# Kernel optimization log

Measured on AMD Instinct MI355X. Metric: run time of the kernel, lower is better.

## Reference

```python
import jax, jax.numpy as jnp
import numpy as np

B, H, F, Z = 256, 2048, 1024, 512
T, PREV, TS = 16, 16, 32  # predicted_visit, previous_visit, time_step


def _relu_dense(x, W, b):
    return jax.nn.relu(x @ W + b)


def setup_inputs() -> dict:
    key = jax.random.key(0)
    ks = jax.random.split(key, 40)
    def rn(i, shape, scale=0.02):
        return jax.random.normal(ks[i], shape, jnp.float32) * scale
    D = H + F + Z  # LSTM input dim: concat(z_j, h_i, y_j_)
    inp = {
        'h_i': jax.random.normal(ks[0], (B, H), jnp.float32),
        # increasing visit times so Hawkes exp(past - current) stays bounded
        'input_t': jnp.cumsum(jax.random.uniform(ks[1], (B, TS), jnp.float32), axis=1) * 0.1,
        'Wk': rn(2, (D, 4 * H)),
        'Wr': rn(3, (H, 4 * H)),
        'b_lstm': jnp.zeros((4 * H,), jnp.float32),
    }
    dense_dims = [(H, F), (F, F), (F, F), (2 * H + 2 * F, Z), (Z, Z), (Z, Z), (2 * H + F, Z), (Z, Z), (Z, Z)]
    for n, (di, do) in enumerate(dense_dims, start=1):
        inp['W%d' % n] = rn(3 + n, (di, do))
        inp['b%d' % n] = jnp.zeros((do,), jnp.float32)
    for n, name in enumerate(['alpha', 'beta', 'base', 'tw']):
        inp[name] = jax.random.uniform(ks[20 + n], (1, 1), jnp.float32) * 0.05
    inp['noise_inf'] = jax.random.normal(ks[30], (T, B, Z), jnp.float32)
    inp['noise_prior'] = jax.random.normal(ks[31], (T, B, Z), jnp.float32)
    return inp


def reference(h_i, input_t, Wk, Wr, b_lstm, W1, b1, W2, b2, W3, b3, W4, b4, W5, b5, W6, b6, W7, b7, W8, b8, W9, b9, alpha, beta, base, tw, noise_inf, noise_prior):
    # ---- Hawkes intensity for every decode step (vectorized over steps) ----
    idxs = PREV + jnp.arange(T)                        # current_time_index per step j
    cur_t = input_t[:, idxs]                           # [B, T]
    diff = input_t[:, None, :] - cur_t[:, :, None]     # [B, T, TS] = past - current
    mask = jnp.arange(TS)[None, None, :] < idxs[None, :, None]
    trig = jnp.sum(jnp.where(mask, jnp.exp(diff), 0.0), axis=-1)   # [B, T]
    lam = base[0, 0] + alpha[0, 0] * beta[0, 0] * trig             # conditional intensity [B, T]
    # original: softplus(matmul(tile(lam,[1,H]), tile(tw,[H,1]))) == softplus(lam * H * tw)
    delta_t = jnp.log1p(jnp.exp(lam * (H * tw[0, 0])))             # [B, T]
    time_est = cur_t + delta_t                                     # [B, T]

    def step(carry, xs):
        h, c, y_prev, z_prev = carry
        lam_j, n_inf, n_pri = xs
        x = jnp.concatenate([z_prev, h_i, y_prev], axis=1)         # [B, Z+H+F]
        gates = x @ Wk + h @ Wr + b_lstm                           # [B, 4H]
        i_g, f_g, g_g, o_g = jnp.split(gates, 4, axis=1)           # keras gate order i,f,c,o
        c_new = jax.nn.sigmoid(f_g) * c + jax.nn.sigmoid(i_g) * jnp.tanh(g_g)
        h_new = jax.nn.sigmoid(o_g) * jnp.tanh(c_new)
        # Original code indexes keras state as c=state[0](=h_new), h_=state[1](=c_new):
        # s_j fed to the VAE nets is the CELL state, and the intensity scales the cell
        # that is carried to the next step, while h carried is the unscaled h_new.
        s_j = c_new
        c_next = lam_j[:, None] * c_new
        y = _relu_dense(_relu_dense(_relu_dense(h_new, W1, b1), W2, b2), W3, b3)
        hz = _relu_dense(jnp.concatenate([h_i, s_j, y, y_prev], axis=1), W4, b4)
        mean = _relu_dense(hz, W5, b5)
        logv = _relu_dense(hz, W6, b6)
        z = mean + n_inf * jnp.sqrt(jnp.exp(logv))
        hz_p = _relu_dense(jnp.concatenate([h_i, s_j, y_prev], axis=1), W7, b7)
        mean_p = _relu_dense(hz_p, W8, b8)
        logv_p = _relu_dense(hz_p, W9, b9)
        z_p = mean_p + n_pri * jnp.sqrt(jnp.exp(logv_p))
        return (h_new, c_next, y, z), (y, mean, logv, z, z_p)

    carry0 = (jnp.zeros((B, H), h_i.dtype), jnp.zeros((B, H), h_i.dtype),
              jnp.zeros((B, F), h_i.dtype), jnp.zeros((B, Z), h_i.dtype))
    xs = (lam.T, noise_inf, noise_prior)  # leading axis = decode step
    _, (ys, means, logvs, zs, zps) = jax.lax.scan(step, carry0, xs)
    tb = lambda a: jnp.transpose(a, (1, 0, 2))    # [T,B,*] -> [B,T,*]
    input_t_all = cur_t.T.reshape(-1, 1)          # matches per-step concat of [B,1]
    time_estimates = time_est.T.reshape(-1, 1)
    return (tb(ys), tb(means), tb(logvs), tb(zs), tb(zps), input_t_all, time_estimates)
```

## Files before the change

### kernel.cpp

```cpp
#include <hip/hip_runtime.h>
#include <stdint.h>

typedef unsigned short u16;
typedef __bf16 bf16x8 __attribute__((ext_vector_type(8)));
typedef float f32x4 __attribute__((ext_vector_type(4)));

static constexpr int NB  = 256;
static constexpr int NH  = 2048;
static constexpr int NF  = 1024;
static constexpr int NZ  = 512;
static constexpr int NT  = 16;
static constexpr int NTS = 32;
static constexpr int NG4 = 8192;
static constexpr int NBLK = 256;

__device__ __forceinline__ u16 f2bf(float f) {
  union { float f; uint32_t u; } x; x.f = f;
  uint32_t r = x.u + 0x7fffu + ((x.u >> 16) & 1u);
  return (u16)(r >> 16);
}
__device__ __forceinline__ float sigm(float x) { return 1.f / (1.f + expf(-x)); }

__device__ __forceinline__ void gload16(const void* g, void* l) {
  __builtin_amdgcn_global_load_lds(
      (__attribute__((address_space(1))) void*)const_cast<void*>(g),
      (__attribute__((address_space(3))) void*)l, 16, 0, 0);
}

__device__ __forceinline__ unsigned aload(const unsigned* p) {
  return __hip_atomic_load(p, __ATOMIC_RELAXED, __HIP_MEMORY_SCOPE_AGENT);
}
__device__ __forceinline__ void astore(unsigned* p, unsigned v) {
  __hip_atomic_store(p, v, __ATOMIC_RELAXED, __HIP_MEMORY_SCOPE_AGENT);
}
__device__ __forceinline__ void t_st(float* p, float v) {
  __hip_atomic_store(p, v, __ATOMIC_RELAXED, __HIP_MEMORY_SCOPE_AGENT);
}
__device__ __forceinline__ void t_st32(uint32_t* p, uint32_t v) {
  __hip_atomic_store(p, v, __ATOMIC_RELAXED, __HIP_MEMORY_SCOPE_AGENT);
}

__device__ __forceinline__ void tl4(const float* p, f32x4& v) {
  asm volatile("global_load_dwordx4 %0, %1, off sc0 sc1" : "=&v"(v) : "v"(p));
}
__device__ __forceinline__ void ts2(void* p, uint32_t lo, uint32_t hi) {
  uint2 d; d.x = lo; d.y = hi;
  asm volatile("global_store_dwordx2 %0, %1, off sc0 sc1" :: "v"(p), "v"(d) : "memory");
}
__device__ __forceinline__ void t_wait() {
  asm volatile("s_waitcnt vmcnt(0)" ::: "memory");
  __builtin_amdgcn_sched_barrier(0);
}

__device__ __forceinline__ void gsync(unsigned* flags, unsigned* rel, unsigned& epoch) {
  ++epoch;
  asm volatile("s_waitcnt vmcnt(0)" ::: "memory");
  __syncthreads();
  if (blockIdx.x == 0) {
    if (threadIdx.x > 0)
      while (aload(&flags[threadIdx.x]) < epoch) __builtin_amdgcn_s_sleep(1);
    __syncthreads();
    if (threadIdx.x == 0) astore(rel, epoch);
  } else if (threadIdx.x == 0) {
    astore(&flags[blockIdx.x], epoch);
    while (aload(rel) < epoch) __builtin_amdgcn_s_sleep(1);
  }
  __syncthreads();
}

template<int F>
__device__ __forceinline__ void gemm_core(const u16* __restrict__ A, const u16* __restrict__ W,
                                          int lda, int ldw, int niter, int wg,
                                          char* lds, f32x4 (&acc)[F][4]) {
  constexpr int BUF = F * 4096 + 4096;
  const int tid = threadIdx.x, lane = tid & 63, wave = tid >> 6;
  const int srow = lane >> 2;
  const int schunk = (((lane & 3) ^ ((lane >> 3) & 3)) << 3);
  const u16* ga = A + (size_t)(wave * (F * 16) + srow) * lda + schunk;
  const u16* gw = W + (size_t)(wave * wg + srow) * ldw + schunk;
  const size_t astep = (size_t)16 * lda;
  auto STAGE = [&](int idx) {
    const int koff = idx << 5;
    char* base = lds + (idx % 3) * BUF;
    char* ad = base + wave * (F * 1024);
#pragma unroll
    for (int k = 0; k < F; ++k) gload16(ga + koff + k * astep, ad + k * 1024);
    gload16(gw + koff, base + F * 4096 + wave * 1024);
  };
  int rA[F], rW[4];
  const int b15 = lane & 15, h4 = lane >> 4, rx = (b15 >> 1) & 3;
#pragma unroll
  for (int f = 0; f < F; ++f) rA[f] = (wave * (F * 16) + f * 16 + b15) * 64 + ((h4 ^ rx) << 4);
#pragma unroll
  for (int q = 0; q < 4; ++q) rW[q] = F * 4096 + (q * 16 + b15) * 64 + ((h4 ^ rx) << 4);

  const int npro = niter < 3 ? niter : 3;
  for (int j = 0; j < npro; ++j) STAGE(j);
  for (int i = 0; i < niter; ++i) {
    const int ahead = niter - 1 - i;
    if constexpr (F == 4) {
      if (ahead >= 2)      asm volatile("s_waitcnt vmcnt(10)" ::: "memory");
      else if (ahead == 1) asm volatile("s_waitcnt vmcnt(5)" ::: "memory");
      else                 asm volatile("s_waitcnt vmcnt(0)" ::: "memory");
    } else if constexpr (F == 2) {
      if (ahead >= 2)      asm volatile("s_waitcnt vmcnt(6)" ::: "memory");
      else if (ahead == 1) asm volatile("s_waitcnt vmcnt(3)" ::: "memory");
      else                 asm volatile("s_waitcnt vmcnt(0)" ::: "memory");
    } else {
      if (ahead >= 2)      asm volatile("s_waitcnt vmcnt(4)" ::: "memory");
      else if (ahead == 1) asm volatile("s_waitcnt vmcnt(2)" ::: "memory");
      else                 asm volatile("s_waitcnt vmcnt(0)" ::: "memory");
    }
    __builtin_amdgcn_sched_barrier(0);
    asm volatile("s_barrier" ::: "memory");
    __builtin_amdgcn_sched_barrier(0);
    const char* base = lds + (i % 3) * BUF;
    bf16x8 av[F], bv[4];
#pragma unroll
    for (int f = 0; f < F; ++f) av[f] = *(const bf16x8*)(base + rA[f]);
#pragma unroll
    for (int q = 0; q < 4; ++q) bv[q] = *(const bf16x8*)(base + rW[q]);
    asm volatile("s_waitcnt lgkmcnt(0)" ::: "memory");
    __builtin_amdgcn_sched_barrier(0);
    asm volatile("s_barrier" ::: "memory");
    __builtin_amdgcn_sched_barrier(0);
    if (i + 3 < niter) STAGE(i + 3);
#pragma unroll
    for (int f = 0; f < F; ++f)
#pragma unroll
      for (int q = 0; q < 4; ++q)
        acc[f][q] = __builtin_amdgcn_mfma_f32_16x16x32_bf16(av[f], bv[q], acc[f][q], 0, 0, 0);
  }
}

__device__ __forceinline__ void flush_u16(const char* tb, u16* dst, int rs, int m0, int n0) {
  __syncthreads();
  const int tid = threadIdx.x, row = tid >> 2, qt = tid & 3;
  const uint2* s = (const uint2*)(tb + row * 128 + qt * 32);
  u16* d = dst + (size_t)(m0 + row) * rs + n0 + qt * 16;
  ts2(d, s[0].x, s[0].y);
  ts2(d + 4, s[1].x, s[1].y);
  ts2(d + 8, s[2].x, s[2].y);
  ts2(d + 12, s[3].x, s[3].y);
}
__device__ __forceinline__ void flush_f32(const char* tb, float* dst, int rs, int m0, int n0) {
  __syncthreads();
  const int tid = threadIdx.x, row = tid >> 2, qt = tid & 3;
  const uint2* s = (const uint2*)(tb + row * 256 + qt * 64);
  float* d = dst + (size_t)(m0 + row) * rs + n0 + qt * 16;
#pragma unroll
  for (int i = 0; i < 8; ++i) ts2(d + i * 2, s[i].x, s[i].y);
}

__device__ __forceinline__ void wbias(float* of, const float* bias, int Nn, int n0,
                                      const f32x4 (&acc)[4][4]) {
  const int tid = threadIdx.x, lane = tid & 63, wave = tid >> 6;
  const int b15 = lane & 15, h4 = lane >> 4;
#pragma unroll
  for (int q = 0; q < 4; ++q) {
    const int n = n0 + q * 16 + b15;
    const float bb = bias[n];
#pragma unroll
    for (int f = 0; f < 4; ++f) {
      const int m = wave * 64 + f * 16 + h4 * 4;
#pragma unroll
      for (int r = 0; r < 4; ++r) t_st(&of[(size_t)(m + r) * Nn + n], acc[f][q][r] + bb);
    }
  }
}

struct TJobs {
  const float* W[13]; u16* D[13];
  int N[13], klo[13], ntx[13], base[14];
  const float* h_i; u16* hi_bf; int hi_base;
};
__global__ __launch_bounds__(256) void setup_tr(TJobs j) {
  const int bid = blockIdx.x, t = threadIdx.x;
  if (bid >= j.hi_base) {
    int i = ((bid - j.hi_base) * 256 + t) * 4;
    float4 v = *(const float4*)(j.h_i + i);
    ushort4 o; o.x = f2bf(v.x); o.y = f2bf(v.y); o.z = f2bf(v.z); o.w = f2bf(v.w);
    *(ushort4*)(j.hi_bf + i) = o;
    return;
  }
  int k = 0;
  while (bid >= j.base[k + 1]) ++k;
  const int tix = bid - j.base[k];
  const int ntx = j.ntx[k];
  const int kk0 = (tix % ntx) * 32, n0 = (tix / ntx) * 32;
  const int N = j.N[k], k_lo = j.klo[k], k_len = ntx * 32;
  const float* W = j.W[k];
  u16* WT = j.D[k];
  __shared__ float tile[32][33];
  const int r = t >> 3, cg = t & 7;
  const float4 v = *(const float4*)(W + (size_t)(k_lo + kk0 + r) * N + n0 + cg * 4);
  tile[r][cg * 4 + 0] = v.x; tile[r][cg * 4 + 1] = v.y;
  tile[r][cg * 4 + 2] = v.z; tile[r][cg * 4 + 3] = v.w;
  __syncthreads();
  ushort4 o;
  o.x = f2bf(tile[cg * 4 + 0][r]);
  o.y = f2bf(tile[cg * 4 + 1][r]);
  o.z = f2bf(tile[cg * 4 + 2][r]);
  o.w = f2bf(tile[cg * 4 + 3][r]);
  *(ushort4*)(WT + (size_t)(n0 + r) * k_len + kk0 + cg * 4) = o;
}

__global__ __launch_bounds__(256) void misc_k(const float* __restrict__ input_t,
                                              const float* alpha, const float* beta,
                                              const float* base_, const float* tw,
                                              const float* b5, const float* b6,
                                              const float* b8, const float* b9,
                                              float* __restrict__ lam_buf,
                                              float* __restrict__ out_it,
                                              float* __restrict__ out_te,
                                              float* __restrict__ bq) {
  const int bid = blockIdx.x, tid = threadIdx.x;
  if (bid < 16) {
    int i = bid * 256 + tid;
    int b = i >> 4, jj = i & 15;
    const float* row = input_t + b * NTS;
    float cur = row[16 + jj];
    float trig = 0.f;
    int lim = 16 + jj;
    for (int s = 0; s < lim; ++s) trig += expf(row[s] - cur);
    float lam = base_[0] + alpha[0] * beta[0] * trig;
    float x = lam * (2048.f * tw[0]);
    float dt = (x > 15.f) ? x : log1pf(expf(x));
    lam_buf[b * NT + jj] = lam;
    out_it[jj * NB + b] = cur;
    out_te[jj * NB + b] = cur + dt;
  } else {
    int i = (bid - 16) * 256 + tid;
    bq[i] = (i < 512) ? b5[i] : (i < 1024) ? b6[i - 512]
          : (i < 1536) ? b8[i - 1024] : b9[i - 1536];
  }
}

struct PArgs {
  const u16 *WkzT, *WkyT, *WkmT, *WrT, *W1T, *W2T, *W3T, *W4T, *W56T, *W7T, *W89T, *hi_bf;
  const float *bl, *b1, *b2, *b3, *b4, *b7, *bq, *ninf, *npri, *lam;
  float *Gc, *H4c, *H7c, *R;
  u16 *hbfV, *zV, *yV, *sbfV, *y1V, *y2V, *hzV, *hzpV;
  float *o_ys, *o_mean, *o_logv, *o_zs, *o_zps;
  unsigned *flags, *rel;
};

__global__ __launch_bounds__(256) void persist(PArgs a) {
  __shared__ __attribute__((aligned(16))) char lds[3 * 20480];
  const int bid = blockIdx.x, tid = threadIdx.x;
  const int lane = tid & 63, wave = tid >> 6, b15 = lane & 15, h4 = lane >> 4;
  unsigned epoch = 0;
  float* Q    = a.R;
  float* Phz  = a.R + (size_t)4 * NB * 512;
  float* Phzp = a.R + (size_t)8 * NB * 512;
  char* tb = lds + 24576;

  const int g_mh = bid >> 7;
  const int g_c0 = (bid & 127) * 16;
  float cR[2][4];
#pragma unroll
  for (int f = 0; f < 2; ++f)
#pragma unroll
    for (int r = 0; r < 4; ++r) cR[f][r] = 0.f;

  {
    if (bid < 144) {
      f32x4 acc[4][4] = {};
      if (bid < 128) {
        const int n0 = bid * 64;
        gemm_core<4>(a.hi_bf, a.WkmT + (size_t)n0 * 2048, 2048, 2048, 64, 16, lds, acc);
        wbias(a.Gc, a.bl, NG4, n0, acc);
      } else if (bid < 136) {
        const int n0 = (bid - 128) * 64;
        gemm_core<4>(a.hi_bf, a.W4T + (size_t)n0 * 6144, 2048, 6144, 64, 16, lds, acc);
        wbias(a.H4c, a.b4, NZ, n0, acc);
      } else {
        const int n0 = (bid - 136) * 64;
        gemm_core<4>(a.hi_bf, a.W7T + (size_t)n0 * 5120, 2048, 5120, 64, 16, lds, acc);
        wbias(a.H7c, a.b7, NZ, n0, acc);
      }
    } else {
      const int zt = (bid - 144) * 256 + tid, nthr = 112 * 256;
      for (int w = zt; w < NB * NH / 2; w += nthr) t_st32((uint32_t*)a.hbfV + w, 0u);
      for (int w = zt; w < NB * NZ / 2; w += nthr) t_st32((uint32_t*)a.zV + w, 0u);
      for (int w = zt; w < NB * NF / 2; w += nthr) t_st32((uint32_t*)a.yV + w, 0u);
    }
    gsync(a.flags, a.rel, epoch);
  }

  float GcR[2][4][4];
#pragma unroll
  for (int f = 0; f < 2; ++f)
#pragma unroll
    for (int q = 0; q < 4; ++q)
#pragma unroll
      for (int r = 0; r < 4; ++r) {
        const int m = g_mh * 128 + wave * 32 + f * 16 + h4 * 4 + r;
        GcR[f][q][r] = a.Gc[(size_t)m * NG4 + q * 2048 + g_c0 + b15];
      }

  for (int t = 0; t < NT; ++t) {
    const u16* hbf_t = a.hbfV + (size_t)t * NB * NH;
    u16* hbf_n = a.hbfV + (size_t)(t + 1) * NB * NH;
    const u16* z_t = a.zV + (size_t)t * NB * NZ;
    u16* z_n = a.zV + (size_t)(t + 1) * NB * NZ;
    const u16* yp = a.yV + (size_t)t * NB * NF;
    u16* yc = a.yV + (size_t)(t + 1) * NB * NF;
    u16* sbf = a.sbfV + (size_t)t * NB * NH;
    u16* y1bf = a.y1V + (size_t)t * NB * NF;
    u16* y2bf = a.y2V + (size_t)t * NB * NF;
    u16* hzbf = a.hzV + (size_t)t * NB * NZ;
    u16* hzpbf = a.hzpV + (size_t)t * NB * NZ;

    {
      f32x4 acc[2][4] = {};
      gemm_core<2>(z_t + (size_t)g_mh * 128 * 512, a.WkzT + (size_t)g_c0 * 512,
                   512, 512, 16, 2048, lds, acc);
      gemm_core<2>(yp + (size_t)g_mh * 128 * 1024, a.WkyT + (size_t)g_c0 * 1024,
                   1024, 1024, 32, 2048, lds, acc);
      gemm_core<2>(hbf_t + (size_t)g_mh * 128 * 2048, a.WrT + (size_t)g_c0 * 2048,
                   2048, 2048, 64, 2048, lds, acc);
      __syncthreads();
      u16* tlh = (u16*)lds;
      u16* tls = (u16*)(lds + 4096);
#pragma unroll
      for (int f = 0; f < 2; ++f)
#pragma unroll
        for (int r = 0; r < 4; ++r) {
          const int ml = wave * 32 + f * 16 + h4 * 4 + r;
          const int m = g_mh * 128 + ml;
          const float ig = acc[f][0][r] + GcR[f][0][r];
          const float fg = acc[f][1][r] + GcR[f][1][r];
          const float gg = acc[f][2][r] + GcR[f][2][r];
          const float og = acc[f][3][r] + GcR[f][3][r];
          const float cn = sigm(fg) * cR[f][r] + sigm(ig) * tanhf(gg);
          const float hn = sigm(og) * tanhf(cn);
          cR[f][r] = a.lam[m * NT + t] * cn;
          tlh[ml * 16 + b15] = f2bf(hn);
          tls[ml * 16 + b15] = f2bf(cn);
        }
      __syncthreads();
      {
        const int row = tid >> 1, half = tid & 1;
        const char* srch = lds + row * 32 + half * 16;
        uint2 u0 = *(const uint2*)srch;
        uint2 u1 = *(const uint2*)(srch + 8);
        u16* dh = hbf_n + (size_t)(g_mh * 128 + row) * NH + g_c0 + half * 8;
        ts2(dh, u0.x, u0.y);
        ts2(dh + 4, u1.x, u1.y);
        const char* srcs = lds + 4096 + row * 32 + half * 16;
        uint2 s0 = *(const uint2*)srcs;
        uint2 s1 = *(const uint2*)(srcs + 8);
        u16* dsp = sbf + (size_t)(g_mh * 128 + row) * NH + g_c0 + half * 8;
        ts2(dsp, s0.x, s0.y);
        ts2(dsp + 4, s1.x, s1.y);
      }
      gsync(a.flags, a.rel, epoch);
    }

    {
      if (bid < 64) {
        const int mt = bid >> 4, nt = bid & 15, m0 = mt * 64, n0 = nt * 64;
        f32x4 acc[1][4] = {};
        gemm_core<1>(hbf_n + (size_t)m0 * 2048, a.W1T + (size_t)n0 * 2048,
                     2048, 2048, 64, 16, lds, acc);
        u16* tl = (u16*)tb;
#pragma unroll
        for (int q = 0; q < 4; ++q) {
          const float bb = a.b1[n0 + q * 16 + b15];
#pragma unroll
          for (int r = 0; r < 4; ++r) {
            const int ml = wave * 16 + h4 * 4 + r;
            tl[ml * 64 + q * 16 + b15] = f2bf(fmaxf(acc[0][q][r] + bb, 0.f));
          }
        }
        flush_u16(tb, y1bf, NF, m0, n0);
      } else if (bid < 128) {
        const int s = bid - 64, mt = s >> 4, rest = s & 15, nt = rest & 7, k = rest >> 3;
        const int m0 = mt * 64, n0 = nt * 64;
        f32x4 acc[1][4] = {};
        gemm_core<1>(sbf + (size_t)m0 * 2048 + k * 1024,
                     a.W4T + 2048 + (size_t)n0 * 6144 + k * 1024,
                     2048, 6144, 32, 16, lds, acc);
        float* tf = (float*)tb;
#pragma unroll
        for (int q = 0; q < 4; ++q)
#pragma unroll
          for (int r = 0; r < 4; ++r)
            tf[(wave * 16 + h4 * 4 + r) * 64 + q * 16 + b15] = acc[0][q][r];
        flush_f32(tb, Phz + (size_t)k * NB * 512, 512, m0, n0);
      } else if (bid < 160) {
        const int s = bid - 128, mt = s >> 3, nt = s & 7, m0 = mt * 64, n0 = nt * 64;
        f32x4 acc[1][4] = {};
        gemm_core<1>(yp + (size_t)m0 * 1024, a.W4T + 5120 + (size_t)n0 * 6144,
                     1024, 6144, 32, 16, lds, acc);
        float* tf = (float*)tb;
#pragma unroll
        for (int q = 0; q < 4; ++q)
#pragma unroll
          for (int r = 0; r < 4; ++r)
            tf[(wave * 16 + h4 * 4 + r) * 64 + q * 16 + b15] = acc[0][q][r];
        flush_f32(tb, Phz + (size_t)2 * NB * 512, 512, m0, n0);
      } else if (bid < 224) {
        const int s = bid - 160, mt = s >> 4, rest = s & 15, nt = rest & 7, k = rest >> 3;
        const int m0 = mt * 64, n0 = nt * 64;
        f32x4 acc[1][4] = {};
        gemm_core<1>(sbf + (size_t)m0 * 2048 + k * 1024,
                     a.W7T + 2048 + (size_t)n0 * 5120 + k * 1024,
                     2048, 5120, 32, 16, lds, acc);
        float* tf = (float*)tb;
#pragma unroll
        for (int q = 0; q < 4; ++q)
#pragma unroll
          for (int r = 0; r < 4; ++r)
            tf[(wave * 16 + h4 * 4 + r) * 64 + q * 16 + b15] = acc[0][q][r];
        flush_f32(tb, Phzp + (size_t)k * NB * 512, 512, m0, n0);
      } else {
        const int s = bid - 224, mt = s >> 3, nt = s & 7, m0 = mt * 64, n0 = nt * 64;
        f32x4 acc[1][4] = {};
        gemm_core<1>(yp + (size_t)m0 * 1024, a.W7T + 4096 + (size_t)n0 * 5120,
                     1024, 5120, 32, 16, lds, acc);
        float* tf = (float*)tb;
#pragma unroll
        for (int q = 0; q < 4; ++q)
#pragma unroll
          for (int r = 0; r < 4; ++r)
            tf[(wave * 16 + h4 * 4 + r) * 64 + q * 16 + b15] = acc[0][q][r];
        flush_f32(tb, Phzp + (size_t)2 * NB * 512, 512, m0, n0);
      }
      gsync(a.flags, a.rel, epoch);
    }

    {
      if (bid < 64) {
        const int mt = bid >> 4, nt = bid & 15, m0 = mt * 64, n0 = nt * 64;
        f32x4 acc[1][4] = {};
        gemm_core<1>(y1bf + (size_t)m0 * 1024, a.W2T + (size_t)n0 * 1024,
                     1024, 1024, 32, 16, lds, acc);
        u16* tl = (u16*)tb;
#pragma unroll
        for (int q = 0; q < 4; ++q) {
          const float bb = a.b2[n0 + q * 16 + b15];
#pragma unroll
          for (int r = 0; r < 4; ++r) {
            const int ml = wave * 16 + h4 * 4 + r;
            tl[ml * 64 + q * 16 + b15] = f2bf(fmaxf(acc[0][q][r] + bb, 0.f));
          }
        }
        flush_u16(tb, y2bf, NF, m0, n0);
      } else if (bid < 96) {
        const int cb = bid - 64;
        for (int p = 0; p < 4; ++p) {
          const int idx = ((p * 32 + cb) * 256 + tid) * 4;
          f32x4 v0, v1, v2;
          tl4(Phzp + idx, v0);
          tl4(Phzp + (size_t)NB * 512 + idx, v1);
          tl4(Phzp + (size_t)2 * NB * 512 + idx, v2);
          f32x4 c0 = *(const f32x4*)(a.H7c + idx);
          t_wait();
          f32x4 v = v0 + v1 + v2 + c0;
          u16 o[4];
#pragma unroll
          for (int r = 0; r < 4; ++r) o[r] = f2bf(fmaxf(v[r], 0.f));
          ts2(hzpbf + idx, (uint32_t)o[0] | ((uint32_t)o[1] << 16),
                           (uint32_t)o[2] | ((uint32_t)o[3] << 16));
        }
      }
      gsync(a.flags, a.rel, epoch);
    }

    {
      if (bid < 64) {
        const int mt = bid >> 4, nt = bid & 15, m0 = mt * 64, n0 = nt * 64;
        f32x4 acc[1][4] = {};
        gemm_core<1>(y2bf + (size_t)m0 * 1024, a.W3T + (size_t)n0 * 1024,
                     1024, 1024, 32, 16, lds, acc);
        u16* tl = (u16*)tb;
#pragma unroll
        for (int q = 0; q < 4; ++q) {
          const int n = n0 + q * 16 + b15;
          const float bb = a.b3[n];
#pragma unroll
          for (int r = 0; r < 4; ++r) {
            const int ml = wave * 16 + h4 * 4 + r;
            const float v = fmaxf(acc[0][q][r] + bb, 0.f);
            tl[ml * 64 + q * 16 + b15] = f2bf(v);
            a.o_ys[((size_t)(m0 + ml) * NT + t) * NF + n] = v;
          }
        }
        flush_u16(tb, yc, NF, m0, n0);
      } else if (bid < 128) {
        const int s = bid - 64, mt = s >> 4, nt = s & 15, m0 = mt * 64, n0 = nt * 64;
        f32x4 acc[1][4] = {};
        gemm_core<1>(hzpbf + (size_t)m0 * 512, a.W89T + (size_t)n0 * 512,
                     512, 512, 16, 16, lds, acc);
        float* tf = (float*)tb;
#pragma unroll
        for (int q = 0; q < 4; ++q) {
          const float bb = a.bq[1024 + n0 + q * 16 + b15];
#pragma unroll
          for (int r = 0; r < 4; ++r)
            tf[(wave * 16 + h4 * 4 + r) * 64 + q * 16 + b15] = fmaxf(acc[0][q][r] + bb, 0.f);
        }
        const int plane = 2 + (n0 >> 9), col0 = n0 & 511;
        flush_f32(tb, Q + (size_t)plane * NB * 512, 512, m0, col0);
      }
      gsync(a.flags, a.rel, epoch);
    }

    {
      if (bid < 32) {
        const int mt = bid >> 3, nt = bid & 7, m0 = mt * 64, n0 = nt * 64;
        f32x4 acc[1][4] = {};
        gemm_core<1>(yc + (size_t)m0 * 1024, a.W4T + 4096 + (size_t)n0 * 6144,
                     1024, 6144, 32, 16, lds, acc);
        float* tf = (float*)tb;
#pragma unroll
        for (int q = 0; q < 4; ++q)
#pragma unroll
          for (int r = 0; r < 4; ++r)
            tf[(wave * 16 + h4 * 4 + r) * 64 + q * 16 + b15] = acc[0][q][r];
        flush_f32(tb, Phz + (size_t)3 * NB * 512, 512, m0, n0);
      }
      gsync(a.flags, a.rel, epoch);
    }

    {
      if (bid < 32) {
        for (int p = 0; p < 4; ++p) {
          const int idx = ((p * 32 + bid) * 256 + tid) * 4;
          f32x4 v0, v1, v2, v3;
          tl4(Phz + idx, v0);
          tl4(Phz + (size_t)NB * 512 + idx, v1);
          tl4(Phz + (size_t)2 * NB * 512 + idx, v2);
          tl4(Phz + (size_t)3 * NB * 512 + idx, v3);
          f32x4 c0 = *(const f32x4*)(a.H4c + idx);
          t_wait();
          f32x4 v = v0 + v1 + v2 + v3 + c0;
          u16 o[4];
#pragma unroll
          for (int r = 0; r < 4; ++r) o[r] = f2bf(fmaxf(v[r], 0.f));
          ts2(hzbf + idx, (uint32_t)o[0] | ((uint32_t)o[1] << 16),
                          (uint32_t)o[2] | ((uint32_t)o[3] << 16));
        }
      }
      gsync(a.flags, a.rel, epoch);
    }

    {
      if (bid < 64) {
        const int mt = bid >> 4, nt = bid & 15, m0 = mt * 64, n0 = nt * 64;
        f32x4 acc[1][4] = {};
        gemm_core<1>(hzbf + (size_t)m0 * 512, a.W56T + (size_t)n0 * 512,
                     512, 512, 16, 16, lds, acc);
        float* tf = (float*)tb;
#pragma unroll
        for (int q = 0; q < 4; ++q) {
          const float bb = a.bq[n0 + q * 16 + b15];
#pragma unroll
          for (int r = 0; r < 4; ++r)
            tf[(wave * 16 + h4 * 4 + r) * 64 + q * 16 + b15] = fmaxf(acc[0][q][r] + bb, 0.f);
        }
        const int plane = n0 >> 9, col0 = n0 & 511;
        flush_f32(tb, Q + (size_t)plane * NB * 512, 512, m0, col0);
      }
      gsync(a.flags, a.rel, epoch);
    }

    {
      if (bid < 128) {
        const int g2 = bid * 256 + tid;
        const int i = g2 * 4, m = i >> 9, jj = i & 511;
        const float* qb = Q + (size_t)m * 512 + jj;
        f32x4 mean, logv, mpv, lpv;
        tl4(qb, mean);
        tl4(qb + (size_t)NB * 512, logv);
        tl4(qb + (size_t)2 * NB * 512, mpv);
        tl4(qb + (size_t)3 * NB * 512, lpv);
        f32x4 nI = *(const f32x4*)(a.ninf + (size_t)t * NB * NZ + i);
        f32x4 nP = *(const f32x4*)(a.npri + (size_t)t * NB * NZ + i);
        t_wait();
        f32x4 z, zp;
        u16 zq[4];
#pragma unroll
        for (int r = 0; r < 4; ++r) {
          z[r] = fmaf(nI[r], sqrtf(expf(logv[r])), mean[r]);
          zp[r] = fmaf(nP[r], sqrtf(expf(lpv[r])), mpv[r]);
          zq[r] = f2bf(z[r]);
        }
        const size_t oo = ((size_t)m * NT + t) * NZ + jj;
        *(f32x4*)(a.o_mean + oo) = mean;
        *(f32x4*)(a.o_logv + oo) = logv;
        *(f32x4*)(a.o_zs + oo) = z;
        *(f32x4*)(a.o_zps + oo) = zp;
        ts2(z_n + i, (uint32_t)zq[0] | ((uint32_t)zq[1] << 16),
                     (uint32_t)zq[2] | ((uint32_t)zq[3] << 16));
      }
      gsync(a.flags, a.rel, epoch);
    }
  }
}

extern "C" void kernel_launch(void* const* d_in, const int* in_sizes, int n_in,
                              void* d_out, int out_size, void* d_ws, size_t ws_size,
                              hipStream_t stream) {
  const float* h_i  = (const float*)d_in[0];
  const float* in_t = (const float*)d_in[1];
  const float* Wk   = (const float*)d_in[2];
  const float* Wr   = (const float*)d_in[3];
  const float* bl   = (const float*)d_in[4];
  const float* W1 = (const float*)d_in[5];  const float* b1 = (const float*)d_in[6];
  const float* W2 = (const float*)d_in[7];  const float* b2 = (const float*)d_in[8];
  const float* W3 = (const float*)d_in[9];  const float* b3 = (const float*)d_in[10];
  const float* W4 = (const float*)d_in[11]; const float* b4 = (const float*)d_in[12];
  const float* W5 = (const float*)d_in[13]; const float* b5 = (const float*)d_in[14];
  const float* W6 = (const float*)d_in[15]; const float* b6 = (const float*)d_in[16];
  const float* W7 = (const float*)d_in[17]; const float* b7 = (const float*)d_in[18];
  const float* W8 = (const float*)d_in[19]; const float* b8 = (const float*)d_in[20];
  const float* W9 = (const float*)d_in[21]; const float* b9 = (const float*)d_in[22];
  const float* alpha = (const float*)d_in[23];
  const float* beta  = (const float*)d_in[24];
  const float* base_ = (const float*)d_in[25];
  const float* tw    = (const float*)d_in[26];
  const float* ninf  = (const float*)d_in[27];
  const float* npri  = (const float*)d_in[28];
  float* out = (float*)d_out;
  (void)in_sizes; (void)n_in; (void)out_size; (void)ws_size;

  char* wsb = (char*)d_ws;
  size_t off = 0;
  auto alloc = [&](size_t bytes) -> void* {
    void* p = wsb + off;
    off += (bytes + 255) & ~(size_t)255;
    return p;
  };
  u16* WkzT = (u16*)alloc((size_t)NG4 * 512 * 2);
  u16* WkmT = (u16*)alloc((size_t)NG4 * 2048 * 2);
  u16* WkyT = (u16*)alloc((size_t)NG4 * 1024 * 2);
  u16* WrT  = (u16*)alloc((size_t)NG4 * NH * 2);
  u16* W1T  = (u16*)alloc((size_t)NF * NH * 2);
  u16* W2T  = (u16*)alloc((size_t)NF * NF * 2);
  u16* W3T  = (u16*)alloc((size_t)NF * NF * 2);
  u16* W4T  = (u16*)alloc((size_t)NZ * 6144 * 2);
  u16* W56T = (u16*)alloc((size_t)1024 * NZ * 2);
  u16* W7T  = (u16*)alloc((size_t)NZ * 5120 * 2);
  u16* W89T = (u16*)alloc((size_t)1024 * NZ * 2);
  u16* hi_bf = (u16*)alloc((size_t)NB * NH * 2);
  float* bq  = (float*)alloc(2048 * 4);
  float* Gc  = (float*)alloc((size_t)NB * NG4 * 4);
  float* H4c = (float*)alloc((size_t)NB * NZ * 4);
  float* H7c = (float*)alloc((size_t)NB * NZ * 4);
  float* lam = (float*)alloc((size_t)NB * NT * 4);
  u16* hbfV = (u16*)alloc((size_t)(NT + 1) * NB * NH * 2);
  u16* zV   = (u16*)alloc((size_t)(NT + 1) * NB * NZ * 2);
  u16* yV   = (u16*)alloc((size_t)(NT + 1) * NB * NF * 2);
  u16* sbfV = (u16*)alloc((size_t)NT * NB * NH * 2);
  u16* y1V  = (u16*)alloc((size_t)NT * NB * NF * 2);
  u16* y2V  = (u16*)alloc((size_t)NT * NB * NF * 2);
  u16* hzV  = (u16*)alloc((size_t)NT * NB * NZ * 2);
  u16* hzpV = (u16*)alloc((size_t)NT * NB * NZ * 2);
  char* zero_start = wsb + off;
  unsigned* bar = (unsigned*)alloc(2048);
  size_t zero_bytes = (size_t)((wsb + off) - zero_start);

  float* out_ys   = out;
  float* out_mean = out_ys + (size_t)NB * NT * NF;
  float* out_logv = out_mean + (size_t)NB * NT * NZ;
  float* out_zs   = out_logv + (size_t)NB * NT * NZ;
  float* out_zps  = out_zs + (size_t)NB * NT * NZ;
  float* out_it   = out_zps + (size_t)NB * NT * NZ;
  float* out_te   = out_it + (size_t)NB * NT;

  hipMemsetAsync(zero_start, 0, zero_bytes, stream);

  TJobs tj{};
  const float* srcs[13] = {Wk, Wk, Wk, Wr, W1, W2, W3, W4, W5, W6, W7, W8, W9};
  u16* dsts[13] = {WkzT, WkmT, WkyT, WrT, W1T, W2T, W3T, W4T,
                   W56T, W56T + (size_t)NZ * NZ, W7T, W89T, W89T + (size_t)NZ * NZ};
  int Ns[13]   = {8192, 8192, 8192, 8192, 1024, 1024, 1024, 512, 512, 512, 512, 512, 512};
  int klos[13] = {0, 512, 2560, 0, 0, 0, 0, 0, 0, 0, 0, 0, 0};
  int klens[13]= {512, 2048, 1024, 2048, 2048, 1024, 1024, 6144, 512, 512, 5120, 512, 512};
  int cum = 0;
  for (int k = 0; k < 13; ++k) {
    tj.W[k] = srcs[k]; tj.D[k] = dsts[k]; tj.N[k] = Ns[k]; tj.klo[k] = klos[k];
    tj.ntx[k] = klens[k] / 32;
    tj.base[k] = cum;
    cum += (klens[k] / 32) * (Ns[k] / 32);
  }
  tj.base[13] = cum;
  tj.h_i = h_i; tj.hi_bf = hi_bf; tj.hi_base = cum;
  const int total_blocks = cum + (NB * NH / 4) / 256;
  setup_tr<<<dim3(total_blocks), dim3(256), 0, stream>>>(tj);

  misc_k<<<dim3(24), dim3(256), 0, stream>>>(in_t, alpha, beta, base_, tw,
                                             b5, b6, b8, b9, lam, out_it, out_te, bq);

  PArgs pa{};
  pa.WkzT = WkzT; pa.WkyT = WkyT; pa.WkmT = WkmT; pa.WrT = WrT;
  pa.W1T = W1T; pa.W2T = W2T; pa.W3T = W3T; pa.W4T = W4T;
  pa.W56T = W56T; pa.W7T = W7T; pa.W89T = W89T; pa.hi_bf = hi_bf;
  pa.bl = bl; pa.b1 = b1; pa.b2 = b2; pa.b3 = b3; pa.b4 = b4; pa.b7 = b7;
  pa.bq = bq; pa.ninf = ninf; pa.npri = npri; pa.lam = lam;
  pa.Gc = Gc; pa.H4c = H4c; pa.H7c = H7c; pa.R = (float*)WkmT;
  pa.hbfV = hbfV; pa.zV = zV; pa.yV = yV; pa.sbfV = sbfV;
  pa.y1V = y1V; pa.y2V = y2V; pa.hzV = hzV; pa.hzpV = hzpV;
  pa.o_ys = out_ys; pa.o_mean = out_mean; pa.o_logv = out_logv;
  pa.o_zs = out_zs; pa.o_zps = out_zps;
  pa.flags = bar; pa.rel = bar + 384;
  persist<<<dim3(NBLK), dim3(256), 0, stream>>>(pa);
}
```

Baseline: 1.723 ms.

## Overlap recurrent h@Wr GEMM with idle blocks in later decode phases

Moves the recurrent h_new @ Wr product for the next step out of the LSTM gate phase. It is split into 512 half-K jobs that run on blocks left idle during the later dense-layer phases, and the partial results are stored as bf16 in a scratch buffer. The next step's gate phase then only adds these precomputed partials, which shortens the critical-path GEMM. It also fuses the hz partial-sum reduction into the W4 GEMM phase, removing one grid barrier. The partials are rounded to bf16, which costs some accuracy, and the extra LDS offsets and scratch aliasing into WkmT add complexity.

```diff
diff --git a/kernel.cpp b/kernel.cpp
--- a/kernel.cpp
+++ b/kernel.cpp
@@ -18,6 +18,9 @@
   union { float f; uint32_t u; } x; x.f = f;
   uint32_t r = x.u + 0x7fffu + ((x.u >> 16) & 1u);
   return (u16)(r >> 16);
+}
+__device__ __forceinline__ float b2f(u16 v) {
+  union { float f; uint32_t u; } c; c.u = (uint32_t)v << 16; return c.f;
 }
 __device__ __forceinline__ float sigm(float x) { return 1.f / (1.f + expf(-x)); }
 
@@ -240,6 +243,7 @@
   const u16 *WkzT, *WkyT, *WkmT, *WrT, *W1T, *W2T, *W3T, *W4T, *W56T, *W7T, *W89T, *hi_bf;
   const float *bl, *b1, *b2, *b3, *b4, *b7, *bq, *ninf, *npri, *lam;
   float *Gc, *H4c, *H7c, *R;
+  u16 *Pgh;
   u16 *hbfV, *zV, *yV, *sbfV, *y1V, *y2V, *hzV, *hzpV;
   float *o_ys, *o_mean, *o_logv, *o_zs, *o_zps;
   unsigned *flags, *rel;
@@ -300,7 +304,6 @@
       }
 
   for (int t = 0; t < NT; ++t) {
-    const u16* hbf_t = a.hbfV + (size_t)t * NB * NH;
     u16* hbf_n = a.hbfV + (size_t)(t + 1) * NB * NH;
     const u16* z_t = a.zV + (size_t)t * NB * NZ;
     u16* z_n = a.zV + (size_t)(t + 1) * NB * NZ;
@@ -312,29 +315,73 @@
     u16* hzbf = a.hzV + (size_t)t * NB * NZ;
     u16* hzpbf = a.hzpV + (size_t)t * NB * NZ;
 
+    auto wr_job = [&](int j) {
+      if (t >= NT - 1) return;
+      const int tile = j & 255, half = j >> 8;
+      const int mh = tile >> 7, c0 = (tile & 127) * 16;
+      f32x4 jac[2][4] = {};
+      gemm_core<2>(hbf_n + (size_t)mh * 128 * 2048 + half * 1024,
+                   a.WrT + (size_t)c0 * 2048 + half * 1024,
+                   2048, 2048, 32, 2048, lds, jac);
+      u16* tlj = (u16*)(lds + 36864);
+#pragma unroll
+      for (int f = 0; f < 2; ++f)
+#pragma unroll
+        for (int q = 0; q < 4; ++q)
+#pragma unroll
+          for (int r = 0; r < 4; ++r)
+            tlj[(wave * 32 + f * 16 + h4 * 4 + r) * 64 + q * 16 + b15] = f2bf(jac[f][q][r]);
+      __syncthreads();
+      u16* dst = a.Pgh + ((size_t)half * 256 + tile) * 8192;
+      const int row = tid >> 1, co = (tid & 1) * 32;
+      const uint2* s = (const uint2*)(lds + 36864 + row * 128 + co * 2);
+      u16* d = dst + row * 64 + co;
+#pragma unroll
+      for (int i = 0; i < 8; ++i) ts2(d + i * 4, s[i].x, s[i].y);
+    };
+
     {
       f32x4 acc[2][4] = {};
       gemm_core<2>(z_t + (size_t)g_mh * 128 * 512, a.WkzT + (size_t)g_c0 * 512,
                    512, 512, 16, 2048, lds, acc);
       gemm_core<2>(yp + (size_t)g_mh * 128 * 1024, a.WkyT + (size_t)g_c0 * 1024,
                    1024, 1024, 32, 2048, lds, acc);
-      gemm_core<2>(hbf_t + (size_t)g_mh * 128 * 2048, a.WrT + (size_t)g_c0 * 2048,
-                   2048, 2048, 64, 2048, lds, acc);
       __syncthreads();
-      u16* tlh = (u16*)lds;
-      u16* tls = (u16*)(lds + 4096);
+      if (t > 0) {
+        const float* t0 = (const float*)(a.Pgh + (size_t)bid * 8192);
+        const float* t1 = (const float*)(a.Pgh + (size_t)(256 + bid) * 8192);
+        f32x4 v0[4], v1[4];
+#pragma unroll
+        for (int i = 0; i < 4; ++i) tl4(t0 + tid * 16 + i * 4, v0[i]);
+#pragma unroll
+        for (int i = 0; i < 4; ++i) tl4(t1 + tid * 16 + i * 4, v1[i]);
+        t_wait();
+        f32x4* l0 = (f32x4*)(lds + tid * 64);
+        f32x4* l1 = (f32x4*)(lds + 16384 + tid * 64);
+#pragma unroll
+        for (int i = 0; i < 4; ++i) { l0[i] = v0[i]; l1[i] = v1[i]; }
+      }
+      __syncthreads();
+      const u16* T0 = (const u16*)lds;
+      const u16* T1 = (const u16*)(lds + 16384);
+      u16* tlh = (u16*)(lds + 36864);
+      u16* tls = (u16*)(lds + 36864 + 4096);
 #pragma unroll
       for (int f = 0; f < 2; ++f)
 #pragma unroll
         for (int r = 0; r < 4; ++r) {
           const int ml = wave * 32 + f * 16 + h4 * 4 + r;
           const int m = g_mh * 128 + ml;
-          const float ig = acc[f][0][r] + GcR[f][0][r];
-          const float fg = acc[f][1][r] + GcR[f][1][r];
-          const float gg = acc[f][2][r] + GcR[f][2][r];
-          const float og = acc[f][3][r] + GcR[f][3][r];
-          const float cn = sigm(fg) * cR[f][r] + sigm(ig) * tanhf(gg);
-          const float hn = sigm(og) * tanhf(cn);
+          float g4[4];
+#pragma unroll
+          for (int q = 0; q < 4; ++q) {
+            float v = acc[f][q][r] + GcR[f][q][r];
+            if (t > 0)
+              v += b2f(T0[ml * 64 + q * 16 + b15]) + b2f(T1[ml * 64 + q * 16 + b15]);
+            g4[q] = v;
+          }
+          const float cn = sigm(g4[1]) * cR[f][r] + sigm(g4[0]) * tanhf(g4[2]);
+          const float hn = sigm(g4[3]) * tanhf(cn);
           cR[f][r] = a.lam[m * NT + t] * cn;
           tlh[ml * 16 + b15] = f2bf(hn);
           tls[ml * 16 + b15] = f2bf(cn);
@@ -342,13 +389,13 @@
       __syncthreads();
       {
         const int row = tid >> 1, half = tid & 1;
-        const char* srch = lds + row * 32 + half * 16;
+        const char* srch = lds + 36864 + row * 32 + half * 16;
         uint2 u0 = *(const uint2*)srch;
         uint2 u1 = *(const uint2*)(srch + 8);
         u16* dh = hbf_n + (size_t)(g_mh * 128 + row) * NH + g_c0 + half * 8;
         ts2(dh, u0.x, u0.y);
         ts2(dh + 4, u1.x, u1.y);
-        const char* srcs = lds + 4096 + row * 32 + half * 16;
+        const char* srcs = lds + 36864 + 4096 + row * 32 + half * 16;
         uint2 s0 = *(const uint2*)srcs;
         uint2 s1 = *(const uint2*)(srcs + 8);
         u16* dsp = sbf + (size_t)(g_mh * 128 + row) * NH + g_c0 + half * 8;
@@ -465,6 +512,8 @@
           ts2(hzpbf + idx, (uint32_t)o[0] | ((uint32_t)o[1] << 16),
                            (uint32_t)o[2] | ((uint32_t)o[3] << 16));
         }
+      } else {
+        wr_job(bid - 96);
       }
       gsync(a.flags, a.rel, epoch);
     }
@@ -504,6 +553,8 @@
         }
         const int plane = 2 + (n0 >> 9), col0 = n0 & 511;
         flush_f32(tb, Q + (size_t)plane * NB * 512, 512, m0, col0);
+      } else {
+        wr_job(160 + bid - 128);
       }
       gsync(a.flags, a.rel, epoch);
     }
@@ -520,29 +571,30 @@
 #pragma unroll
           for (int r = 0; r < 4; ++r)
             tf[(wave * 16 + h4 * 4 + r) * 64 + q * 16 + b15] = acc[0][q][r];
-        flush_f32(tb, Phz + (size_t)3 * NB * 512, 512, m0, n0);
-      }
-      gsync(a.flags, a.rel, epoch);
-    }
-
-    {
-      if (bid < 32) {
-        for (int p = 0; p < 4; ++p) {
-          const int idx = ((p * 32 + bid) * 256 + tid) * 4;
-          f32x4 v0, v1, v2, v3;
-          tl4(Phz + idx, v0);
-          tl4(Phz + (size_t)NB * 512 + idx, v1);
-          tl4(Phz + (size_t)2 * NB * 512 + idx, v2);
-          tl4(Phz + (size_t)3 * NB * 512 + idx, v3);
-          f32x4 c0 = *(const f32x4*)(a.H4c + idx);
-          t_wait();
-          f32x4 v = v0 + v1 + v2 + v3 + c0;
+        __syncthreads();
+        const int row = tid >> 2, qt = tid & 3;
+        const size_t base = (size_t)(m0 + row) * 512 + n0 + qt * 16;
+        f32x4 p0[4], p1[4], p2[4];
+#pragma unroll
+        for (int i = 0; i < 4; ++i) {
+          tl4(Phz + base + i * 4, p0[i]);
+          tl4(Phz + (size_t)NB * 512 + base + i * 4, p1[i]);
+          tl4(Phz + (size_t)2 * NB * 512 + base + i * 4, p2[i]);
+        }
+        t_wait();
+#pragma unroll
+        for (int i = 0; i < 4; ++i) {
+          f32x4 v = *(const f32x4*)(tf + row * 64 + qt * 16 + i * 4)
+                  + p0[i] + p1[i] + p2[i]
+                  + *(const f32x4*)(a.H4c + base + i * 4);
           u16 o[4];
 #pragma unroll
           for (int r = 0; r < 4; ++r) o[r] = f2bf(fmaxf(v[r], 0.f));
-          ts2(hzbf + idx, (uint32_t)o[0] | ((uint32_t)o[1] << 16),
-                          (uint32_t)o[2] | ((uint32_t)o[3] << 16));
-        }
+          ts2(hzbf + base + i * 4, (uint32_t)o[0] | ((uint32_t)o[1] << 16),
+                                   (uint32_t)o[2] | ((uint32_t)o[3] << 16));
+        }
+      } else {
+        wr_job(288 + bid - 32);
       }
       gsync(a.flags, a.rel, epoch);
     }
@@ -702,6 +754,7 @@
   pa.bl = bl; pa.b1 = b1; pa.b2 = b2; pa.b3 = b3; pa.b4 = b4; pa.b7 = b7;
   pa.bq = bq; pa.ninf = ninf; pa.npri = npri; pa.lam = lam;
   pa.Gc = Gc; pa.H4c = H4c; pa.H7c = H7c; pa.R = (float*)WkmT;
+  pa.Pgh = (u16*)((float*)WkmT + (size_t)11 * NB * 512);
   pa.hbfV = hbfV; pa.zV = zV; pa.yV = yV; pa.sbfV = sbfV;
   pa.y1V = y1V; pa.y2V = y2V; pa.hzV = hzV; pa.hzpV = hzpV;
   pa.o_ys = out_ys; pa.o_mean = out_mean; pa.o_logv = out_logv;
```

New measurement: 1.709 ms (median of 4 runs). Within noise of the previous version (-0.8%).
